# Kernel tuning notes

Hardware: AMD Instinct MI355X
Metric: run time of the kernel (lower is better)

Reference implementation:

```python
import jax, jax.numpy as jnp
import numpy as np

L, D, H, DH, FF, V, NL = 12, 768, 12, 64, 3072, 32000, 2
B, Q = 8, 512
EPS = 1e-12
SCALE = 1.0 / (DH ** 0.5)


def setup_inputs() -> dict:
    key = jax.random.key(0)
    ks = jax.random.split(key, 16)
    s = 0.02
    nrm = lambda k, shape: jax.random.normal(k, shape, jnp.float32) * s
    return {
        "tox": jax.random.randint(ks[0], (B, Q), 0, V),
        "ntox": jax.random.randint(ks[1], (B, Q), 0, V),
        "attn_mask": jnp.ones((B, Q), jnp.float32),
        "word_emb": nrm(ks[2], (V, D)),
        "q_w": nrm(ks[3], (L, D, H, DH)),
        "k_w": nrm(ks[4], (L, D, H, DH)),
        "v_w": nrm(ks[5], (L, D, H, DH)),
        "o_w": nrm(ks[6], (L, D, H, DH)),
        "r_w": nrm(ks[7], (L, D, H, DH)),
        "r_w_bias": nrm(ks[8], (L, H, DH)),
        "r_r_bias": nrm(ks[9], (L, H, DH)),
        "ln1_g": jnp.ones((L, D), jnp.float32),
        "ln1_b": jnp.zeros((L, D), jnp.float32),
        "ff_w1": nrm(ks[10], (L, D, FF)),
        "ff_b1": jnp.zeros((L, FF), jnp.float32),
        "ff_w2": nrm(ks[11], (L, FF, D)),
        "ff_b2": jnp.zeros((L, D), jnp.float32),
        "ln2_g": jnp.ones((L, D), jnp.float32),
        "ln2_b": jnp.zeros((L, D), jnp.float32),
        "sum_w": nrm(ks[12], (D, D)),
        "sum_b": jnp.zeros((D,), jnp.float32),
        "proj_w": nrm(ks[13], (D, NL)),
        "proj_b": jnp.zeros((NL,), jnp.float32),
    }


def _layer_norm(x, g, b):
    m = x.mean(-1, keepdims=True)
    v = ((x - m) ** 2).mean(-1, keepdims=True)
    return (x - m) / jnp.sqrt(v + EPS) * g + b


def _rel_shift(x, klen):
    # HF XLNet rel_shift_bnij: x is [b, n, i, j] with j = qlen + klen
    b, n, i, j = x.shape
    x = x.reshape(b, n, j, i)[:, :, 1:, :].reshape(b, n, i, j - 1)
    return x[:, :, :, :klen]


def _pos_encoding(qlen, klen, d):
    # positions klen .. -(qlen-1), sinusoidal -> [qlen+klen, d]
    inv_freq = 1.0 / (10000.0 ** (jnp.arange(0, d, 2, dtype=jnp.float32) / d))
    pos = jnp.arange(klen, -qlen, -1.0, dtype=jnp.float32)
    sinu = pos[:, None] * inv_freq[None, :]
    return jnp.concatenate([jnp.sin(sinu), jnp.cos(sinu)], axis=-1)


def _forward(ids, attn_mask, word_emb, q_w, k_w, v_w, o_w, r_w, r_w_bias, r_r_bias,
             ln1_g, ln1_b, ff_w1, ff_b1, ff_w2, ff_b2, ln2_g, ln2_b,
             sum_w, sum_b, proj_w, proj_b):
    qlen = ids.shape[1]
    # masks (HF semantics: 1 = masked-out). non_tgt_mask always allows the diagonal.
    am = attn_mask.T                                   # [K, B], 1 = keep
    data_mask = (1.0 - am)[None]                       # [1, K, B]
    am4 = (data_mask[:, :, :, None] > 0).astype(jnp.float32)   # [1, K, B, 1]
    eye = jnp.eye(qlen, dtype=jnp.float32)[:, :, None, None]
    non_tgt = ((am4 - eye) > 0).astype(jnp.float32)    # [Q, K, B, 1]
    mask_bnij = jnp.transpose(non_tgt, (2, 3, 0, 1))   # [B, 1, Q, K]

    h = word_emb[ids.T]                                # [Q, B, D]
    r = _pos_encoding(qlen, qlen, D)                   # [2Q, D]

    for l in range(L):
        qh = jnp.einsum('ibh,hnd->ibnd', h, q_w[l])
        kh = jnp.einsum('ibh,hnd->ibnd', h, k_w[l])
        vh = jnp.einsum('ibh,hnd->ibnd', h, v_w[l])
        kr = jnp.einsum('jh,hnd->jnd', r, r_w[l])
        ac = jnp.einsum('ibnd,jbnd->bnij', qh + r_w_bias[l], kh)
        bd = jnp.einsum('ibnd,jnd->bnij', qh + r_r_bias[l], kr)
        bd = _rel_shift(bd, qlen)
        score = (ac + bd) * SCALE - 1e30 * mask_bnij
        prob = jax.nn.softmax(score, axis=-1)
        vec = jnp.einsum('bnij,jbnd->ibnd', prob, vh)
        attn_out = jnp.einsum('ibnd,hnd->ibh', vec, o_w[l])
        h = _layer_norm(attn_out + h, ln1_g[l], ln1_b[l])
        ff = jax.nn.gelu(h @ ff_w1[l] + ff_b1[l], approximate=False) @ ff_w2[l] + ff_b2[l]
        h = _layer_norm(h + ff, ln2_g[l], ln2_b[l])

    out = jnp.transpose(h, (1, 0, 2))                  # [B, Q, D]
    last = out[:, -1]                                  # SequenceSummary 'last'
    summ = jnp.tanh(last @ sum_w + sum_b)
    return summ @ proj_w + proj_b                      # [B, NL]


def reference(tox, ntox, attn_mask, word_emb, q_w, k_w, v_w, o_w, r_w, r_w_bias, r_r_bias,
              ln1_g, ln1_b, ff_w1, ff_b1, ff_w2, ff_b2, ln2_g, ln2_b,
              sum_w, sum_b, proj_w, proj_b):
    # ntox stream is computed then discarded in the original forward (dead code);
    # the returned logits depend only on the tox stream.
    return _forward(tox, attn_mask, word_emb, q_w, k_w, v_w, o_w, r_w, r_w_bias, r_r_bias,
                    ln1_g, ln1_b, ff_w1, ff_b1, ff_w2, ff_b2, ln2_g, ln2_b,
                    sum_w, sum_b, proj_w, proj_b)
```

## Files before the change

### kernel.cpp

```cpp
#include <hip/hip_runtime.h>
#include <math.h>
#include <stdint.h>

#define LAYERS 12
#define DMODEL 768
#define NHEAD 12
#define DHEAD 64
#define DFF 3072
#define BATCH 8
#define SEQ 512
#define NTOK (BATCH*SEQ)
#define KLEN 1024
#define SCALE 0.125f

typedef __bf16 bf16x8 __attribute__((ext_vector_type(8)));
typedef __bf16 bf16x4v __attribute__((ext_vector_type(4)));
typedef float f32x4 __attribute__((ext_vector_type(4)));

__device__ __forceinline__ void gld16(const void* g, void* l) {
  auto gp = reinterpret_cast<const __attribute__((address_space(1))) void*>(
      reinterpret_cast<uintptr_t>(g));
  auto lp = reinterpret_cast<__attribute__((address_space(3))) void*>(
      reinterpret_cast<uintptr_t>(l));
  __builtin_amdgcn_global_load_lds(gp, lp, 16, 0, 0);
}

__global__ void k_embed(const int* __restrict__ tox, const float* __restrict__ emb,
                        float* __restrict__ h, __bf16* __restrict__ hb) {
  int n = blockIdx.x;
  int i = n >> 3, b = n & 7;
  int tok = tox[b*SEQ + i];
  const float* src = emb + (size_t)tok * DMODEL;
  size_t off = (size_t)n * DMODEL;
  for (int d = threadIdx.x; d < DMODEL; d += blockDim.x) {
    float v = src[d];
    h[off+d] = v; hb[off+d] = (__bf16)v;
  }
}

__global__ void k_posenc(__bf16* __restrict__ r) {
  int idx = blockIdx.x * blockDim.x + threadIdx.x;
  if (idx >= KLEN * DMODEL) return;
  int k = idx / DMODEL, d = idx % DMODEL;
  float pos = (float)(SEQ - k);
  int j = (d < 384) ? d : d - 384;
  float invf = powf(10000.0f, -(2.0f * (float)j) / 768.0f);
  float a = pos * invf;
  r[idx] = (__bf16)((d < 384) ? sinf(a) : cosf(a));
}

__global__ __launch_bounds__(256) void k_wt(const float* __restrict__ src, __bf16* __restrict__ dst,
                                            int srcN, int dstK, long sstride, long dstride, int drowoff) {
  __shared__ float t[32][33];
  int nt = blockIdx.x, kt = blockIdx.y, l = blockIdx.z;
  const float* s = src + (size_t)l * sstride;
  __bf16* d = dst + (size_t)l * dstride;
  int r = threadIdx.x >> 3, c4 = (threadIdx.x & 7) * 4;
  float4 v = *(const float4*)&s[(size_t)(kt*32 + r)*srcN + nt*32 + c4];
  t[r][c4+0]=v.x; t[r][c4+1]=v.y; t[r][c4+2]=v.z; t[r][c4+3]=v.w;
  __syncthreads();
  bf16x4v o = { (__bf16)t[c4+0][r], (__bf16)t[c4+1][r], (__bf16)t[c4+2][r], (__bf16)t[c4+3][r] };
  *(bf16x4v*)&d[(size_t)(drowoff + nt*32 + r)*dstK + kt*32 + c4] = o;
}

__global__ void k_cvt(const float* __restrict__ s, __bf16* __restrict__ d, int n4) {
  int i = blockIdx.x*256 + threadIdx.x;
  if (i >= n4) return;
  float4 v = ((const float4*)s)[i];
  bf16x4v o = { (__bf16)v.x, (__bf16)v.y, (__bf16)v.z, (__bf16)v.w };
  ((bf16x4v*)d)[i] = o;
}

__global__ __launch_bounds__(256) void k_vt(const __bf16* __restrict__ vb, __bf16* __restrict__ vtg) {
  __shared__ __bf16 t[32][36];
  int it = blockIdx.x, dt = blockIdx.y, bn = blockIdx.z;
  int b = bn / 12, n = bn % 12;
  int r = threadIdx.x >> 3, c4 = (threadIdx.x & 7) * 4;
  bf16x4v v = *(const bf16x4v*)&vb[((size_t)(it*32 + r)*8 + b)*768 + n*64 + dt*32 + c4];
  t[r][c4+0]=v[0]; t[r][c4+1]=v[1]; t[r][c4+2]=v[2]; t[r][c4+3]=v[3];
  __syncthreads();
  bf16x4v o = { t[c4+0][r], t[c4+1][r], t[c4+2][r], t[c4+3][r] };
  *(bf16x4v*)&vtg[((size_t)bn*64 + dt*32 + r)*512 + it*32 + c4] = o;
}

template<int ACT, int OUTM, int SPLITK>
__global__ __launch_bounds__(256) void k_mgemm(
    const __bf16* __restrict__ A, const __bf16* __restrict__ B,
    const float* __restrict__ bias, void* __restrict__ Cv,
    __bf16* __restrict__ q1, __bf16* __restrict__ q2,
    __bf16* __restrict__ kk, __bf16* __restrict__ vv,
    const float* __restrict__ rwbp, const float* __restrict__ rrbp,
    int M, int N, int K, long bz, long cz) {
  __shared__ __align__(16) __bf16 As[128*32];
  __shared__ __align__(16) __bf16 Bs[128*32];
  int tid = threadIdx.x;
  int wave = tid >> 6, lane = tid & 63;
  int lr = lane & 15, lc = lane >> 4;
  int wm = wave >> 1, wn = wave & 1;
  int m0 = blockIdx.y * 128, n0 = blockIdx.x * 128;
  const __bf16* Bp = B + (SPLITK > 1 ? 0 : (size_t)blockIdx.z * bz);
  int kbeg = (SPLITK > 1) ? blockIdx.z * (K/SPLITK) : 0;
  int kend = (SPLITK > 1) ? kbeg + K/SPLITK : K;

  f32x4 acc[4][4];
  #pragma unroll
  for (int i = 0; i < 4; ++i)
    #pragma unroll
    for (int j = 0; j < 4; ++j) acc[i][j] = f32x4{0.f,0.f,0.f,0.f};

  int q0 = tid, q1i = 256 + tid;
  int r0 = q0 >> 2, s0 = (q0 & 3) ^ (r0 & 3);
  int r1 = q1i >> 2, s1 = (q1i & 3) ^ (r1 & 3);
  char* As0 = (char*)As + (size_t)wave*1024;
  char* Bs0 = (char*)Bs + (size_t)wave*1024;

  for (int k0 = kbeg; k0 < kend; k0 += 32) {
    __syncthreads();
    gld16(A  + (size_t)(m0 + r0)*K + k0 + s0*8, As0);
    gld16(A  + (size_t)(m0 + r1)*K + k0 + s1*8, As0 + 4096);
    gld16(Bp + (size_t)(n0 + r0)*K + k0 + s0*8, Bs0);
    gld16(Bp + (size_t)(n0 + r1)*K + k0 + s1*8, Bs0 + 4096);
    __syncthreads();
    bf16x8 af[4], bfr[4];
    #pragma unroll
    for (int mi = 0; mi < 4; ++mi) {
      int row = wm*64 + mi*16 + lr;
      af[mi] = *(const bf16x8*)((const char*)As + row*64 + ((lc ^ (row & 3))*16));
    }
    #pragma unroll
    for (int ni = 0; ni < 4; ++ni) {
      int row = wn*64 + ni*16 + lr;
      bfr[ni] = *(const bf16x8*)((const char*)Bs + row*64 + ((lc ^ (row & 3))*16));
    }
    #pragma unroll
    for (int mi = 0; mi < 4; ++mi)
      #pragma unroll
      for (int ni = 0; ni < 4; ++ni)
        acc[mi][ni] = __builtin_amdgcn_mfma_f32_16x16x32_bf16(af[mi], bfr[ni], acc[mi][ni], 0, 0, 0);
  }

  #pragma unroll
  for (int mi = 0; mi < 4; ++mi) {
    #pragma unroll
    for (int ni = 0; ni < 4; ++ni) {
      int gn = n0 + wn*64 + ni*16 + lr;
      float bv = (bias && (SPLITK == 1 || blockIdx.z == 0)) ? bias[gn] : 0.f;
      #pragma unroll
      for (int j = 0; j < 4; ++j) {
        int gm = m0 + wm*64 + mi*16 + lc*4 + j;
        float v = acc[mi][ni][j] + bv;
        if (ACT == 1) v = 0.5f*v*(1.0f + erff(v*0.70710678118654752f));
        if (OUTM == 0) {
          ((float*)Cv)[(size_t)blockIdx.z*cz + (size_t)gm*N + gn] = v;
        } else if (OUTM == 1) {
          ((__bf16*)Cv)[(size_t)blockIdx.z*cz + (size_t)gm*N + gn] = (__bf16)v;
        } else {
          if (gn < 768) {
            size_t o = (size_t)gm*768 + gn;
            q1[o] = (__bf16)(v + rwbp[gn]);
            q2[o] = (__bf16)(v + rrbp[gn]);
          } else if (gn < 1536) {
            kk[(size_t)gm*768 + gn - 768] = (__bf16)v;
          } else {
            vv[(size_t)gm*768 + gn - 1536] = (__bf16)v;
          }
        }
      }
    }
  }
}

__global__ __launch_bounds__(256) void k_pv(
    const __bf16* __restrict__ qrw, const __bf16* __restrict__ qrr,
    const __bf16* __restrict__ kb, const __bf16* __restrict__ vtg,
    const __bf16* __restrict__ krb, __bf16* __restrict__ vec) {
  __shared__ __align__(16) char lds[49664];
  int tid = threadIdx.x;
  int w = tid >> 6, lane = tid & 63;
  int lr = lane & 15, lg = lane >> 4;
  int bn = blockIdx.y;
  int b = bn / 12, n = bn % 12;
  int i0 = blockIdx.x * 64;
  char* KT = lds;
  char* VT = lds + 8192;
  char* KR = lds + 16384;
  char* BD = lds + 32768;
  char* Plds = lds + 41472 + w*2048;

  #pragma unroll
  for (int c = 0; c < 2; ++c) {
    int id = c*256 + tid;
    int row = id >> 3, cc = (id & 7) ^ (row & 7);
    gld16(qrw + ((size_t)(i0 + row)*8 + b)*768 + n*64 + cc*8, KT + c*4096 + w*1024);
    gld16(qrr + ((size_t)(i0 + row)*8 + b)*768 + n*64 + cc*8, VT + c*4096 + w*1024);
  }
  __syncthreads();
  bf16x8 qwf[2], qrf[2];
  #pragma unroll
  for (int ks = 0; ks < 2; ++ks) {
    int row = w*16 + lr;
    qwf[ks] = *(const bf16x8*)(KT + row*128 + (((lg + ks*4) ^ (row & 7))*16));
    qrf[ks] = *(const bf16x8*)(VT + row*128 + (((lg + ks*4) ^ (row & 7))*16));
  }

  f32x4 O[4];
  #pragma unroll
  for (int d = 0; d < 4; ++d) O[d] = f32x4{0.f,0.f,0.f,0.f};
  float m_run = -1e30f, den = 0.f;

  for (int jt = 0; jt < 8; ++jt) {
    int j0 = jt * 64;
    int kw0 = j0 - i0 + 449;
    __syncthreads();
    #pragma unroll
    for (int c = 0; c < 2; ++c) {
      int id = c*256 + tid;
      int row = id >> 3, cc = (id & 7) ^ (row & 7);
      gld16(kb + ((size_t)(j0 + row)*8 + b)*768 + n*64 + cc*8, KT + c*4096 + w*1024);
      gld16(vtg + ((size_t)bn*64 + row)*512 + j0 + cc*8, VT + c*4096 + w*1024);
    }
    #pragma unroll
    for (int c = 0; c < 4; ++c) {
      int id = c*256 + tid;
      int row = id >> 3, cc = (id & 7) ^ (row & 7);
      gld16(krb + (size_t)(kw0 + row)*768 + n*64 + cc*8, KR + c*4096 + w*1024);
    }
    __syncthreads();

    __builtin_amdgcn_s_setprio(1);
    f32x4 acf[4];
    #pragma unroll
    for (int ksub = 0; ksub < 4; ++ksub) acf[ksub] = f32x4{0.f,0.f,0.f,0.f};
    #pragma unroll
    for (int ks = 0; ks < 2; ++ks) {
      #pragma unroll
      for (int ksub = 0; ksub < 4; ++ksub) {
        int row = ksub*16 + lr;
        bf16x8 kf = *(const bf16x8*)(KT + row*128 + (((lg + ks*4) ^ (row & 7))*16));
        acf[ksub] = __builtin_amdgcn_mfma_f32_16x16x32_bf16(kf, qwf[ks], acf[ksub], 0, 0, 0);
      }
    }
    #pragma unroll
    for (int kt = 0; kt < 8; ++kt) {
      f32x4 bda = f32x4{0.f,0.f,0.f,0.f};
      #pragma unroll
      for (int ks = 0; ks < 2; ++ks) {
        int rowk = kt*16 + lr;
        bf16x8 krf = *(const bf16x8*)(KR + rowk*128 + (((lg + ks*4) ^ (rowk & 7))*16));
        bda = __builtin_amdgcn_mfma_f32_16x16x32_bf16(qrf[ks], krf, bda, 0, 0, 0);
      }
      #pragma unroll
      for (int jreg = 0; jreg < 4; ++jreg) {
        int il = w*16 + lg*4 + jreg;
        int jloc = kt*16 + lr + il - 63;
        if ((unsigned)jloc < 64u)
          *(__bf16*)(BD + (il*68 + jloc)*2) = (__bf16)bda[jreg];
      }
    }
    __builtin_amdgcn_s_setprio(0);

    float sc[4][4];
    float mt = -1e30f;
    int qrow = w*16 + lr;
    #pragma unroll
    for (int ksub = 0; ksub < 4; ++ksub) {
      bf16x4v bdv = *(const bf16x4v*)(BD + (qrow*68 + ksub*16 + lg*4)*2);
      #pragma unroll
      for (int r = 0; r < 4; ++r) {
        float s = (acf[ksub][r] + (float)bdv[r]) * SCALE;
        sc[ksub][r] = s;
        mt = fmaxf(mt, s);
      }
    }
    mt = fmaxf(mt, __shfl_xor(mt, 16));
    mt = fmaxf(mt, __shfl_xor(mt, 32));
    float m_new = fmaxf(m_run, mt);
    float f = __expf(m_run - m_new);
    m_run = m_new;
    float psum = 0.f;
    #pragma unroll
    for (int ksub = 0; ksub < 4; ++ksub) {
      bf16x4v pv;
      #pragma unroll
      for (int r = 0; r < 4; ++r) {
        float p = __expf(sc[ksub][r] - m_new);
        psum += p;
        pv[r] = (__bf16)p;
      }
      int k = ksub*16 + lg*4;
      *(bf16x4v*)(Plds + lr*128 + (((k >> 3) ^ (lr & 7))*16) + (k & 7)*2) = pv;
    }
    den = den*f + psum;
    float fv[4];
    #pragma unroll
    for (int j = 0; j < 4; ++j) fv[j] = __shfl(f, lg*4 + j);
    #pragma unroll
    for (int d = 0; d < 4; ++d)
      #pragma unroll
      for (int j = 0; j < 4; ++j) O[d][j] *= fv[j];
    __builtin_amdgcn_s_setprio(1);
    #pragma unroll
    for (int ks = 0; ks < 2; ++ks) {
      bf16x8 paf = *(const bf16x8*)(Plds + lr*128 + (((lg + ks*4) ^ (lr & 7))*16));
      #pragma unroll
      for (int d = 0; d < 4; ++d) {
        int row = d*16 + lr;
        bf16x8 vf = *(const bf16x8*)(VT + row*128 + (((lg + ks*4) ^ (row & 7))*16));
        O[d] = __builtin_amdgcn_mfma_f32_16x16x32_bf16(paf, vf, O[d], 0, 0, 0);
      }
    }
    __builtin_amdgcn_s_setprio(0);
  }

  den += __shfl_xor(den, 16);
  den += __shfl_xor(den, 32);
  float inv = 1.0f / den;
  float iv[4];
  #pragma unroll
  for (int j = 0; j < 4; ++j) iv[j] = __shfl(inv, lg*4 + j);
  #pragma unroll
  for (int d = 0; d < 4; ++d) {
    #pragma unroll
    for (int j = 0; j < 4; ++j) {
      int qg = i0 + w*16 + lg*4 + j;
      int dd = d*16 + lr;
      vec[((size_t)qg*8 + b)*768 + n*64 + dd] = (__bf16)(O[d][j] * iv[j]);
    }
  }
}

__global__ __launch_bounds__(256) void k_head1(
    const float* __restrict__ last, const float* __restrict__ sumw,
    const float* __restrict__ sumb, float* __restrict__ summ) {
  __shared__ float red[256];
  int tid = threadIdx.x;
  int nn = blockIdx.x*16 + (tid & 15);
  int r = (tid >> 4) & 7;
  int half = tid >> 7;
  const float* lp = last + (size_t)r*768 + half*384;
  const float* wp = sumw + (size_t)half*384*768 + nn;
  float s = 0.f;
  #pragma unroll 4
  for (int k = 0; k < 384; ++k) s += lp[k] * wp[(size_t)k*768];
  red[tid] = s;
  __syncthreads();
  if (tid < 128) {
    float t = red[tid] + red[tid + 128];
    summ[(size_t)r*768 + nn] = tanhf(t + sumb[nn]);
  }
}

__global__ __launch_bounds__(128) void k_head2(
    const float* __restrict__ summ, const float* __restrict__ pjw,
    const float* __restrict__ pjb, float* __restrict__ out) {
  __shared__ float red[128];
  int tid = threadIdx.x;
  int o = tid & 15;
  int r = o >> 1, c = o & 1;
  int seg = tid >> 4;
  float s = 0.f;
  #pragma unroll 4
  for (int k = seg*96; k < seg*96 + 96; ++k) s += summ[(size_t)r*768 + k] * pjw[(size_t)k*2 + c];
  red[tid] = s;
  __syncthreads();
  if (tid < 16) {
    float t = 0.f;
    #pragma unroll
    for (int sg = 0; sg < 8; ++sg) t += red[sg*16 + tid];
    out[tid] = t + pjb[tid & 1];
  }
}

template<int HASX2>
__global__ __launch_bounds__(192) void k_ln_res(
    const float* __restrict__ x, const float* __restrict__ x2,
    const float* __restrict__ res, const float* __restrict__ g,
    const float* __restrict__ bta, float* __restrict__ out, __bf16* __restrict__ outb) {
  __shared__ float red[6];
  int row = blockIdx.x, tid = threadIdx.x;
  size_t off = (size_t)row*768 + tid*4;
  float4 v = *(const float4*)(x + off);
  if (HASX2) {
    float4 u = *(const float4*)(x2 + off);
    v.x += u.x; v.y += u.y; v.z += u.z; v.w += u.w;
  }
  {
    float4 u = *(const float4*)(res + off);
    v.x += u.x; v.y += u.y; v.z += u.z; v.w += u.w;
  }
  float s = v.x + v.y + v.z + v.w;
  #pragma unroll
  for (int o = 32; o; o >>= 1) s += __shfl_down(s, o, 64);
  if ((tid & 63) == 0) red[tid >> 6] = s;
  __syncthreads();
  float mean = (red[0] + red[1] + red[2]) * (1.0f/768.0f);
  float a0 = v.x - mean, a1 = v.y - mean, a2 = v.z - mean, a3 = v.w - mean;
  float vs = a0*a0 + a1*a1 + a2*a2 + a3*a3;
  #pragma unroll
  for (int o = 32; o; o >>= 1) vs += __shfl_down(vs, o, 64);
  if ((tid & 63) == 0) red[3 + (tid >> 6)] = vs;
  __syncthreads();
  float var = (red[3] + red[4] + red[5]) * (1.0f/768.0f);
  float rstd = 1.0f / sqrtf(var + 1e-12f);
  float4 gv = *(const float4*)(g + tid*4);
  float4 bv = *(const float4*)(bta + tid*4);
  float4 y;
  y.x = a0*rstd*gv.x + bv.x;
  y.y = a1*rstd*gv.y + bv.y;
  y.z = a2*rstd*gv.z + bv.z;
  y.w = a3*rstd*gv.w + bv.w;
  *(float4*)(out + off) = y;
  bf16x4v yb = { (__bf16)y.x, (__bf16)y.y, (__bf16)y.z, (__bf16)y.w };
  *(bf16x4v*)(outb + off) = yb;
}

extern "C" void kernel_launch(void* const* d_in, const int* in_sizes, int n_in,
                              void* d_out, int out_size, void* d_ws, size_t ws_size,
                              hipStream_t stream) {
  (void)in_sizes; (void)n_in; (void)out_size; (void)ws_size;
  const int*   tox  = (const int*)d_in[0];
  const float* emb  = (const float*)d_in[3];
  const float* q_w  = (const float*)d_in[4];
  const float* k_w  = (const float*)d_in[5];
  const float* v_w  = (const float*)d_in[6];
  const float* o_w  = (const float*)d_in[7];
  const float* r_w  = (const float*)d_in[8];
  const float* rwb  = (const float*)d_in[9];
  const float* rrb  = (const float*)d_in[10];
  const float* ln1g = (const float*)d_in[11];
  const float* ln1b = (const float*)d_in[12];
  const float* fw1  = (const float*)d_in[13];
  const float* fb1  = (const float*)d_in[14];
  const float* fw2  = (const float*)d_in[15];
  const float* fb2  = (const float*)d_in[16];
  const float* ln2g = (const float*)d_in[17];
  const float* ln2b = (const float*)d_in[18];
  const float* sumw = (const float*)d_in[19];
  const float* sumb = (const float*)d_in[20];
  const float* pjw  = (const float*)d_in[21];
  const float* pjb  = (const float*)d_in[22];
  float* out = (float*)d_out;

  char* wsp = (char*)d_ws;
  auto alloc = [&](size_t bytes) { char* rp = wsp; wsp += (bytes + 255) & ~(size_t)255; return rp; };
  __bf16* qkvw   = (__bf16*)alloc((size_t)LAYERS*2304*768*2);
  __bf16* rwt    = (__bf16*)alloc((size_t)LAYERS*768*768*2);
  __bf16* owb    = (__bf16*)alloc((size_t)LAYERS*768*768*2);
  __bf16* ff1t   = (__bf16*)alloc((size_t)LAYERS*768*3072*2);
  __bf16* ff2t   = (__bf16*)alloc((size_t)LAYERS*3072*768*2);
  float*  h      = (float*) alloc((size_t)NTOK*DMODEL*4);
  __bf16* h_bf   = (__bf16*)alloc((size_t)NTOK*DMODEL*2);
  __bf16* r_bf   = (__bf16*)alloc((size_t)KLEN*DMODEL*2);
  __bf16* krb    = (__bf16*)alloc(((size_t)LAYERS*KLEN + 8)*DMODEL*2);
  __bf16* vtg    = (__bf16*)alloc((size_t)96*64*512*2);
  __bf16* vec_bf = (__bf16*)alloc((size_t)NTOK*DMODEL*2);
  float*  A5     = (float*) alloc((size_t)2*NTOK*DMODEL*4);
  float*  summ   = (float*) alloc((size_t)BATCH*DMODEL*4);
  char*   U      = alloc((size_t)NTOK*DMODEL*2 * 4);
  __bf16* qrw    = (__bf16*)U;
  __bf16* qrr    = (__bf16*)(U + (size_t)NTOK*DMODEL*2);
  __bf16* kbuf   = (__bf16*)(U + (size_t)NTOK*DMODEL*2*2);
  __bf16* vb     = (__bf16*)(U + (size_t)NTOK*DMODEL*2*3);
  __bf16* mid_bf = (__bf16*)U;

  dim3 b256(256);
  k_wt<<<dim3(24,24,LAYERS), b256, 0, stream>>>(q_w, qkvw, 768, 768, 589824, 2304*768, 0);
  k_wt<<<dim3(24,24,LAYERS), b256, 0, stream>>>(k_w, qkvw, 768, 768, 589824, 2304*768, 768);
  k_wt<<<dim3(24,24,LAYERS), b256, 0, stream>>>(v_w, qkvw, 768, 768, 589824, 2304*768, 1536);
  k_wt<<<dim3(24,24,LAYERS), b256, 0, stream>>>(r_w, rwt, 768, 768, 589824, 589824, 0);
  k_wt<<<dim3(96,24,LAYERS), b256, 0, stream>>>(fw1, ff1t, 3072, 768, (long)768*3072, (long)3072*768, 0);
  k_wt<<<dim3(24,96,LAYERS), b256, 0, stream>>>(fw2, ff2t, 768, 3072, (long)3072*768, (long)768*3072, 0);
  k_cvt<<<(LAYERS*589824/4 + 255)/256, b256, 0, stream>>>(o_w, owb, LAYERS*589824/4);

  k_embed<<<NTOK, b256, 0, stream>>>(tox, emb, h, h_bf);
  k_posenc<<<(KLEN*DMODEL + 255)/256, b256, 0, stream>>>(r_bf);

  k_mgemm<0,1,1><<<dim3(6,8,LAYERS), b256, 0, stream>>>(r_bf, rwt, nullptr, krb,
      nullptr, nullptr, nullptr, nullptr, nullptr, nullptr,
      KLEN, 768, 768, (long)589824, (long)KLEN*DMODEL);

  for (int l = 0; l < LAYERS; ++l) {
    k_mgemm<0,2,1><<<dim3(18,32), b256, 0, stream>>>(h_bf, qkvw + (size_t)l*2304*768, nullptr, nullptr,
        qrw, qrr, kbuf, vb, rwb + l*DMODEL, rrb + l*DMODEL, NTOK, 2304, 768, 0, 0);
    k_vt<<<dim3(16,2,96), b256, 0, stream>>>(vb, vtg);
    k_pv<<<dim3(8,96), b256, 0, stream>>>(qrw, qrr, kbuf, vtg,
        krb + (size_t)l*KLEN*DMODEL, vec_bf);
    k_mgemm<0,0,1><<<dim3(6,32), b256, 0, stream>>>(vec_bf, owb + (size_t)l*589824, nullptr, A5,
        nullptr, nullptr, nullptr, nullptr, nullptr, nullptr, NTOK, 768, 768, 0, 0);
    k_ln_res<0><<<NTOK, dim3(192), 0, stream>>>(A5, nullptr, h, ln1g + l*DMODEL, ln1b + l*DMODEL, h, h_bf);
    k_mgemm<1,1,1><<<dim3(24,32), b256, 0, stream>>>(h_bf, ff1t + (size_t)l*768*3072, fb1 + (size_t)l*DFF, mid_bf,
        nullptr, nullptr, nullptr, nullptr, nullptr, nullptr, NTOK, DFF, 768, 0, 0);
    k_mgemm<0,0,2><<<dim3(6,32,2), b256, 0, stream>>>(mid_bf, ff2t + (size_t)l*3072*768, fb2 + l*DMODEL, A5,
        nullptr, nullptr, nullptr, nullptr, nullptr, nullptr, NTOK, 768, DFF, 0, (long)NTOK*DMODEL);
    k_ln_res<1><<<NTOK, dim3(192), 0, stream>>>(A5, A5 + (size_t)NTOK*DMODEL, h,
        ln2g + l*DMODEL, ln2b + l*DMODEL, h, h_bf);
  }

  const float* lastp = h + (size_t)(NTOK - BATCH)*DMODEL;
  k_head1<<<dim3(48), b256, 0, stream>>>(lastp, sumw, sumb, summ);
  k_head2<<<dim3(1), dim3(128), 0, stream>>>(summ, pjw, pjb, out);
}
```

Before: 2.639 ms.

## Double GEMM k-tile to 64 and reuse sliding positional-key window in attention

The generic MFMA GEMM now stages 64-wide K slices per iteration with an 8-way XOR swizzle, which halves the number of barrier pairs per output tile but doubles LDS use. The attention kernel keeps the 128-row positional-key window as a ring buffer, loading only the 64 new rows per key tile instead of all 128. Each wave now computes only the 5 of 8 positional sub-tiles that can land in the valid band for its rows. Together these cut global traffic and skip wasted MFMA work, at the cost of more LDS per block and more complex index arithmetic.

```diff
diff --git a/kernel.cpp b/kernel.cpp
--- a/kernel.cpp
+++ b/kernel.cpp
@@ -91,8 +91,8 @@
     __bf16* __restrict__ kk, __bf16* __restrict__ vv,
     const float* __restrict__ rwbp, const float* __restrict__ rrbp,
     int M, int N, int K, long bz, long cz) {
-  __shared__ __align__(16) __bf16 As[128*32];
-  __shared__ __align__(16) __bf16 Bs[128*32];
+  __shared__ __align__(16) __bf16 As[128*64];
+  __shared__ __align__(16) __bf16 Bs[128*64];
   int tid = threadIdx.x;
   int wave = tid >> 6, lane = tid & 63;
   int lr = lane & 15, lc = lane >> 4;
@@ -108,35 +108,44 @@
     #pragma unroll
     for (int j = 0; j < 4; ++j) acc[i][j] = f32x4{0.f,0.f,0.f,0.f};
 
-  int q0 = tid, q1i = 256 + tid;
-  int r0 = q0 >> 2, s0 = (q0 & 3) ^ (r0 & 3);
-  int r1 = q1i >> 2, s1 = (q1i & 3) ^ (r1 & 3);
-  char* As0 = (char*)As + (size_t)wave*1024;
-  char* Bs0 = (char*)Bs + (size_t)wave*1024;
-
-  for (int k0 = kbeg; k0 < kend; k0 += 32) {
+  int srow[4], scc[4];
+  #pragma unroll
+  for (int c = 0; c < 4; ++c) {
+    int id = c*256 + tid;
+    srow[c] = id >> 3;
+    scc[c]  = (id & 7) ^ (srow[c] & 7);
+  }
+
+  for (int k0 = kbeg; k0 < kend; k0 += 64) {
     __syncthreads();
-    gld16(A  + (size_t)(m0 + r0)*K + k0 + s0*8, As0);
-    gld16(A  + (size_t)(m0 + r1)*K + k0 + s1*8, As0 + 4096);
-    gld16(Bp + (size_t)(n0 + r0)*K + k0 + s0*8, Bs0);
-    gld16(Bp + (size_t)(n0 + r1)*K + k0 + s1*8, Bs0 + 4096);
+    #pragma unroll
+    for (int c = 0; c < 4; ++c)
+      gld16(A + (size_t)(m0 + srow[c])*K + k0 + scc[c]*8,
+            (char*)As + c*4096 + wave*1024);
+    #pragma unroll
+    for (int c = 0; c < 4; ++c)
+      gld16(Bp + (size_t)(n0 + srow[c])*K + k0 + scc[c]*8,
+            (char*)Bs + c*4096 + wave*1024);
     __syncthreads();
-    bf16x8 af[4], bfr[4];
-    #pragma unroll
-    for (int mi = 0; mi < 4; ++mi) {
-      int row = wm*64 + mi*16 + lr;
-      af[mi] = *(const bf16x8*)((const char*)As + row*64 + ((lc ^ (row & 3))*16));
-    }
-    #pragma unroll
-    for (int ni = 0; ni < 4; ++ni) {
-      int row = wn*64 + ni*16 + lr;
-      bfr[ni] = *(const bf16x8*)((const char*)Bs + row*64 + ((lc ^ (row & 3))*16));
-    }
-    #pragma unroll
-    for (int mi = 0; mi < 4; ++mi)
-      #pragma unroll
-      for (int ni = 0; ni < 4; ++ni)
-        acc[mi][ni] = __builtin_amdgcn_mfma_f32_16x16x32_bf16(af[mi], bfr[ni], acc[mi][ni], 0, 0, 0);
+    #pragma unroll
+    for (int ks = 0; ks < 2; ++ks) {
+      bf16x8 af[4], bfr[4];
+      #pragma unroll
+      for (int mi = 0; mi < 4; ++mi) {
+        int row = wm*64 + mi*16 + lr;
+        af[mi] = *(const bf16x8*)((const char*)As + row*128 + (((lc + ks*4) ^ (row & 7))*16));
+      }
+      #pragma unroll
+      for (int ni = 0; ni < 4; ++ni) {
+        int row = wn*64 + ni*16 + lr;
+        bfr[ni] = *(const bf16x8*)((const char*)Bs + row*128 + (((lc + ks*4) ^ (row & 7))*16));
+      }
+      #pragma unroll
+      for (int mi = 0; mi < 4; ++mi)
+        #pragma unroll
+        for (int ni = 0; ni < 4; ++ni)
+          acc[mi][ni] = __builtin_amdgcn_mfma_f32_16x16x32_bf16(af[mi], bfr[ni], acc[mi][ni], 0, 0, 0);
+    }
   }
 
   #pragma unroll
@@ -186,6 +195,7 @@
   char* KR = lds + 16384;
   char* BD = lds + 32768;
   char* Plds = lds + 41472 + w*2048;
+  int base449 = 449 - i0;
 
   #pragma unroll
   for (int c = 0; c < 2; ++c) {
@@ -194,6 +204,12 @@
     gld16(qrw + ((size_t)(i0 + row)*8 + b)*768 + n*64 + cc*8, KT + c*4096 + w*1024);
     gld16(qrr + ((size_t)(i0 + row)*8 + b)*768 + n*64 + cc*8, VT + c*4096 + w*1024);
   }
+  #pragma unroll
+  for (int c = 0; c < 4; ++c) {
+    int id = c*256 + tid;
+    int row = id >> 3, cc = (id & 7) ^ (row & 7);
+    gld16(krb + (size_t)(base449 + row)*768 + n*64 + cc*8, KR + c*4096 + w*1024);
+  }
   __syncthreads();
   bf16x8 qwf[2], qrf[2];
   #pragma unroll
@@ -210,7 +226,6 @@
 
   for (int jt = 0; jt < 8; ++jt) {
     int j0 = jt * 64;
-    int kw0 = j0 - i0 + 449;
     __syncthreads();
     #pragma unroll
     for (int c = 0; c < 2; ++c) {
@@ -219,11 +234,16 @@
       gld16(kb + ((size_t)(j0 + row)*8 + b)*768 + n*64 + cc*8, KT + c*4096 + w*1024);
       gld16(vtg + ((size_t)bn*64 + row)*512 + j0 + cc*8, VT + c*4096 + w*1024);
     }
-    #pragma unroll
-    for (int c = 0; c < 4; ++c) {
-      int id = c*256 + tid;
-      int row = id >> 3, cc = (id & 7) ^ (row & 7);
-      gld16(krb + (size_t)(kw0 + row)*768 + n*64 + cc*8, KR + c*4096 + w*1024);
+    if (jt) {
+      int sb = (64*(jt+1)) & 127;
+      #pragma unroll
+      for (int c = 0; c < 2; ++c) {
+        int id = c*256 + tid;
+        int rw = id >> 3;
+        int cc = (id & 7) ^ (rw & 7);
+        gld16(krb + (size_t)(base449 + 64*jt + 64 + rw)*768 + n*64 + cc*8,
+              KR + sb*128 + c*4096 + w*1024);
+      }
     }
     __syncthreads();
 
@@ -240,13 +260,16 @@
         acf[ksub] = __builtin_amdgcn_mfma_f32_16x16x32_bf16(kf, qwf[ks], acf[ksub], 0, 0, 0);
       }
     }
-    #pragma unroll
-    for (int kt = 0; kt < 8; ++kt) {
+    int ktbase = 3 - w;
+    #pragma unroll
+    for (int t = 0; t < 5; ++t) {
+      int kt = ktbase + t;
       f32x4 bda = f32x4{0.f,0.f,0.f,0.f};
       #pragma unroll
       for (int ks = 0; ks < 2; ++ks) {
         int rowk = kt*16 + lr;
-        bf16x8 krf = *(const bf16x8*)(KR + rowk*128 + (((lg + ks*4) ^ (rowk & 7))*16));
+        int s = (64*jt + rowk) & 127;
+        bf16x8 krf = *(const bf16x8*)(KR + s*128 + (((lg + ks*4) ^ (rowk & 7))*16));
         bda = __builtin_amdgcn_mfma_f32_16x16x32_bf16(qrf[ks], krf, bda, 0, 0, 0);
       }
       #pragma unroll
```

Result: faster. 2.341 ms (-11.3%).
